# Performance work log

Hardware: AMD Instinct MI355X
Metric: run time of the kernel (lower is better)

## Reference

```python
import jax, jax.numpy as jnp
import numpy as np

N, E, DIN, H, CHID, COUT, S = 20000, 320000, 128, 4, 64, 64, 32
EPS_BN = 1e-5


def setup_inputs() -> dict:
    key = jax.random.key(0)
    ks = jax.random.split(key, 20)
    g = lambda k, shp, s=0.1: jax.random.normal(k, shp, dtype=jnp.float32) * s
    return {
        "x": jax.random.normal(ks[0], (N, DIN), dtype=jnp.float32),
        "edge_index": jax.random.randint(ks[1], (2, E), 0, N, dtype=jnp.int32),
        "struct_feat": jax.random.normal(ks[2], (N, S), dtype=jnp.float32),
        # GATConv (layer 1)
        "W1": g(ks[3], (H * CHID, DIN)),
        "att_src1": g(ks[4], (1, H, CHID)),
        "att_dst1": g(ks[5], (1, H, CHID)),
        "bias1": jnp.zeros((CHID,), jnp.float32),
        # HybridGateGATLayer (layer 2)
        "W2": g(ks[6], (H * COUT, CHID)),
        "att_src2": g(ks[7], (1, H, COUT)),
        "att_dst2": g(ks[8], (1, H, COUT)),
        "bias2": jnp.zeros((COUT,), jnp.float32),
        "Wt": g(ks[9], (1, S)),
        "bt": jnp.zeros((1,), jnp.float32),
        "We1": g(ks[10], (8, 4), 0.5),
        "be1": jnp.zeros((8,), jnp.float32),
        "We2": g(ks[11], (1, 8), 0.5),
        "be2": jnp.zeros((1,), jnp.float32),
        "betas": jnp.array([1.15, 0.85, 0.1, 0.08, 0.12], jnp.float32),
    }


def _seg_softmax(logits, seg, n):
    m = jax.ops.segment_max(logits, seg, num_segments=n)
    m = jnp.where(jnp.isfinite(m), m, 0.0)
    ex = jnp.exp(logits - m[seg])
    s = jax.ops.segment_sum(ex, seg, num_segments=n)
    return ex / (s[seg] + 1e-16)


def _cos(a, b):
    na = jnp.maximum(jnp.linalg.norm(a, axis=-1), 1e-8)
    nb = jnp.maximum(jnp.linalg.norm(b, axis=-1), 1e-8)
    return (a * b).sum(-1) / (na * nb)


def reference(x, edge_index, struct_feat, W1, att_src1, att_dst1, bias1,
              W2, att_src2, att_dst2, bias2, Wt, bt, We1, be1, We2, be2, betas):
    n = x.shape[0]
    src0, dst0 = edge_index[0], edge_index[1]
    # ---- layer 1: standard GATConv with self loops, concat=False (head mean) ----
    loop = jnp.arange(n, dtype=src0.dtype)
    src = jnp.concatenate([src0, loop])
    dst = jnp.concatenate([dst0, loop])
    h = (x @ W1.T).reshape(n, H, CHID)
    a_s = (h * att_src1).sum(-1)  # [N,H]
    a_d = (h * att_dst1).sum(-1)
    al = jax.nn.leaky_relu(a_s[src] + a_d[dst], 0.2)  # [E+N,H]
    alpha1 = _seg_softmax(al, dst, n)
    out1 = jax.ops.segment_sum(h[src] * alpha1[..., None], dst, num_segments=n)
    h1 = jax.nn.relu(out1.mean(1) + bias1)  # [N,CHID]
    # batch norm (affine=False, batch stats, biased var)
    mu = h1.mean(0)
    var = ((h1 - mu) ** 2).mean(0)
    h1 = (h1 - mu) / jnp.sqrt(var + EPS_BN)
    # ---- layer 2: HybridGateGATLayer (no self loops) ----
    x2 = (h1 @ W2.T).reshape(n, H, COUT)
    node_trust = jax.nn.sigmoid(struct_feat @ Wt.T + bt).squeeze(-1)  # [N]
    as2 = (x2 * att_src2).sum(-1)
    ad2 = (x2 * att_dst2).sum(-1)
    j, i = src0, dst0
    alpha_raw = jax.nn.leaky_relu(as2[j] + ad2[i], 0.2)  # [E,H]
    struct_sim = _cos(struct_feat[j], struct_feat[i])  # [E]
    xf = x2.reshape(n, H * COUT)
    feat_sim = _cos(xf[j], xf[i])
    agreement = struct_sim * feat_sim
    conflict = jnp.abs(struct_sim - feat_sim)
    cues = jnp.stack([struct_sim, feat_sim, agreement, conflict], axis=-1)  # [E,4]
    gate = (jax.nn.relu(cues @ We1.T + be1) @ We2.T + be2).squeeze(-1)
    edge_bonus = jax.nn.sigmoid(gate) * jax.nn.relu(agreement)
    edge_trust = jnp.sqrt(jnp.clip(node_trust[j] * node_trust[i], 0.0))
    trust_bonus = edge_trust * jax.nn.relu(0.5 * (struct_sim + feat_sim))
    gate_logit = (betas[0] * struct_sim + betas[1] * feat_sim + betas[2] * agreement
                  + betas[3] * edge_bonus + betas[4] * trust_bonus)
    alpha2 = _seg_softmax(alpha_raw + gate_logit[:, None], i, n)  # [E,H]
    out2 = jax.ops.segment_sum(x2[j] * alpha2[..., None], i, num_segments=n)
    return out2.mean(1) + bias2  # [N,COUT]
```

## Files before the change

kernel.cpp:

```cpp
#include <hip/hip_runtime.h>
#include <hip/hip_bf16.h>
#include <hip/hip_fp16.h>

#define C_DIN 128
#define C_H 4
#define C_CH 64
#define C_HC 256
#define C_S 32
#define ACH 32
#define MBLK 64
#define XROW 264

typedef __attribute__((ext_vector_type(8))) _Float16 half8;
typedef __attribute__((ext_vector_type(4))) float f32x4;

__device__ __forceinline__ float lrelu(float x) { return x >= 0.f ? x : 0.2f * x; }

__device__ __forceinline__ float sub_sum32(float v) {
#pragma unroll
    for (int off = 16; off > 0; off >>= 1) v += __shfl_xor(v, off);
    return v;
}

__global__ void k_count(const int* __restrict__ dst, int* __restrict__ deg, int E) {
    int e = blockIdx.x * blockDim.x + threadIdx.x;
    if (e < E) atomicAdd(&deg[dst[e]], 1);
}

__global__ void k_scan(const int* __restrict__ deg, int* __restrict__ row_ptr,
                       int* __restrict__ cursor, int n) {
    __shared__ int part[1024];
    int t = threadIdx.x;
    const int C = (n + 1023) / 1024;
    int base = t * C;
    int s = 0;
    for (int k = 0; k < C; ++k) {
        int idx = base + k;
        if (idx < n) s += deg[idx];
    }
    part[t] = s;
    __syncthreads();
    for (int off = 1; off < 1024; off <<= 1) {
        int v = (t >= off) ? part[t - off] : 0;
        __syncthreads();
        part[t] += v;
        __syncthreads();
    }
    int run = (t == 0) ? 0 : part[t - 1];
    for (int k = 0; k < C; ++k) {
        int idx = base + k;
        if (idx < n) { row_ptr[idx] = run; cursor[idx] = run; run += deg[idx]; }
    }
    if (t == 1023) row_ptr[n] = run;
}

__global__ void k_scatter(const int* __restrict__ src, const int* __restrict__ dst,
                          int* __restrict__ cursor, int* __restrict__ adj_src, int E) {
    int e = blockIdx.x * blockDim.x + threadIdx.x;
    if (e < E) {
        int d = dst[e];
        int p = atomicAdd(&cursor[d], 1);
        adj_src[p] = src[e];
    }
}

__global__ __launch_bounds__(256) void k_gemm1(
    const float* __restrict__ x, const float* __restrict__ W1,
    const float* __restrict__ att_s, const float* __restrict__ att_d,
    __half* __restrict__ hh_out, float* __restrict__ a_s, float* __restrict__ a_d, int n) {
    __shared__ __align__(16) _Float16 bs[4 * 16 * 64 * 8];
    __shared__ __align__(16) _Float16 as_[4 * 4 * 64 * 8];
    int t = threadIdx.x;
    int r0 = blockIdx.x * MBLK;
    {
        int c = t;
        const float4* wrow = (const float4*)(W1 + (size_t)c * C_DIN);
        int nt = c >> 4, cl = c & 15;
#pragma unroll
        for (int ch = 0; ch < 16; ++ch) {
            float4 f0 = wrow[ch * 2], f1 = wrow[ch * 2 + 1];
            int ks = ch >> 2, lg = ch & 3;
            _Float16* dst = &bs[(((ks * 16 + nt) * 64) + (lg * 16 + cl)) * 8];
            dst[0] = (_Float16)f0.x; dst[1] = (_Float16)f0.y;
            dst[2] = (_Float16)f0.z; dst[3] = (_Float16)f0.w;
            dst[4] = (_Float16)f1.x; dst[5] = (_Float16)f1.y;
            dst[6] = (_Float16)f1.z; dst[7] = (_Float16)f1.w;
        }
    }
    {
        int row = t >> 2, q = t & 3;
        int rr = r0 + row;
        int mt = row >> 4, rl = row & 15;
        const float4* xrow = (const float4*)(x + (size_t)rr * C_DIN);
#pragma unroll
        for (int cc = 0; cc < 4; ++cc) {
            int ch = q * 4 + cc;
            float4 f0 = make_float4(0, 0, 0, 0), f1 = make_float4(0, 0, 0, 0);
            if (rr < n) { f0 = xrow[ch * 2]; f1 = xrow[ch * 2 + 1]; }
            int ks = ch >> 2, lg = ch & 3;
            _Float16* dst = &as_[(((ks * 4 + mt) * 64) + (lg * 16 + rl)) * 8];
            dst[0] = (_Float16)f0.x; dst[1] = (_Float16)f0.y;
            dst[2] = (_Float16)f0.z; dst[3] = (_Float16)f0.w;
            dst[4] = (_Float16)f1.x; dst[5] = (_Float16)f1.y;
            dst[6] = (_Float16)f1.z; dst[7] = (_Float16)f1.w;
        }
    }
    __syncthreads();
    int w = t >> 6, l = t & 63;
    f32x4 acc[4][4];
#pragma unroll
    for (int mt = 0; mt < 4; ++mt)
#pragma unroll
        for (int nt = 0; nt < 4; ++nt) acc[mt][nt] = (f32x4){0.f, 0.f, 0.f, 0.f};
#pragma unroll
    for (int ks = 0; ks < 4; ++ks) {
        half8 af[4], bf[4];
#pragma unroll
        for (int mt = 0; mt < 4; ++mt)
            af[mt] = *(const half8*)&as_[(((ks * 4 + mt) * 64) + l) * 8];
#pragma unroll
        for (int nt = 0; nt < 4; ++nt)
            bf[nt] = *(const half8*)&bs[(((ks * 16 + (w * 4 + nt)) * 64) + l) * 8];
#pragma unroll
        for (int mt = 0; mt < 4; ++mt)
#pragma unroll
            for (int nt = 0; nt < 4; ++nt)
                acc[mt][nt] = __builtin_amdgcn_mfma_f32_16x16x32_f16(af[mt], bf[nt],
                                                                     acc[mt][nt], 0, 0, 0);
    }
    int cl = l & 15, rg = l >> 4;
    float atv_s[4], atv_d[4];
#pragma unroll
    for (int nt = 0; nt < 4; ++nt) {
        atv_s[nt] = att_s[w * 64 + nt * 16 + cl];
        atv_d[nt] = att_d[w * 64 + nt * 16 + cl];
    }
#pragma unroll
    for (int mt = 0; mt < 4; ++mt) {
#pragma unroll
        for (int r = 0; r < 4; ++r) {
            int rr = r0 + mt * 16 + rg * 4 + r;
            float vs = 0.f, vd = 0.f;
#pragma unroll
            for (int nt = 0; nt < 4; ++nt) {
                float v = acc[mt][nt][r];
                vs += atv_s[nt] * v;
                vd += atv_d[nt] * v;
                if (rr < n)
                    hh_out[(size_t)rr * C_HC + w * 64 + nt * 16 + cl] = __float2half(v);
            }
#pragma unroll
            for (int off = 1; off < 16; off <<= 1) {
                vs += __shfl_xor(vs, off);
                vd += __shfl_xor(vd, off);
            }
            if (cl == 0 && rr < n) { a_s[rr * C_H + w] = vs; a_d[rr * C_H + w] = vd; }
        }
    }
}

__global__ void k_layer1(const int* __restrict__ row_ptr, const int* __restrict__ adj_src,
                         const __half* __restrict__ hhlf, const float* __restrict__ a_s,
                         const float* __restrict__ a_d, const float* __restrict__ bias1,
                         float* __restrict__ h1) {
    int d = blockIdx.x;
    int t = threadIdx.x, hh = t >> 5, cp = t & 31;
    int beg = row_ptr[d], end = row_ptr[d + 1];
    float adh = a_d[d * C_H + hh];
    float p_self = expf(lrelu(a_s[d * C_H + hh] + adh));
    __shared__ float alpha_l[C_H][ACH];
    __shared__ int src_l[ACH];
    const __half2* selfrow = (const __half2*)(hhlf + (size_t)d * C_HC + hh * 64);
    float2 sv = __half22float2(selfrow[cp]);
    float accx = p_self * sv.x, accy = p_self * sv.y;
    float s_part = (cp == 0) ? p_self : 0.f;
    for (int cbeg = beg; cbeg < end; cbeg += ACH) {
        int cn = min(end - cbeg, ACH);
        __syncthreads();
        if (cp < cn) {
            int s = adj_src[cbeg + cp];
            if (hh == 0) src_l[cp] = s;
            float p = expf(lrelu(a_s[s * C_H + hh] + adh));
            alpha_l[hh][cp] = p;
            s_part += p;
        }
        __syncthreads();
        for (int i = 0; i < cn; ++i) {
            int s = src_l[i];
            float a = alpha_l[hh][i];
            float2 v = __half22float2(
                *(const __half2*)(hhlf + (size_t)s * C_HC + hh * 64 + cp * 2));
            accx += a * v.x;
            accy += a * v.y;
        }
    }
    float s = sub_sum32(s_part);
    float inv = 1.f / (s + 1e-16f);
    __shared__ float2 red[128];
    red[t] = make_float2(accx * inv, accy * inv);
    __syncthreads();
    if (t < 32) {
        float2 r0 = red[t], r1 = red[t + 32], r2 = red[t + 64], r3 = red[t + 96];
        float2 b = *(const float2*)&bias1[t * 2];
        float vx = (r0.x + r1.x + r2.x + r3.x) * 0.25f + b.x;
        float vy = (r0.y + r1.y + r2.y + r3.y) * 0.25f + b.y;
        *(float2*)&h1[(size_t)d * C_CH + t * 2] =
            make_float2(fmaxf(vx, 0.f), fmaxf(vy, 0.f));
    }
}

__global__ void k_bnstats(const float* __restrict__ h1, float* __restrict__ bn, int n) {
    int t = threadIdx.x;
    int c = t & 63, rg = t >> 6;
    float s = 0.f, s2 = 0.f;
    for (int r = blockIdx.x * 4 + rg; r < n; r += gridDim.x * 4) {
        float v = h1[(size_t)r * C_CH + c];
        s += v;
        s2 += v * v;
    }
    __shared__ float ls[256], ls2[256];
    ls[t] = s; ls2[t] = s2;
    __syncthreads();
    if (t < 64) {
        s = ls[t] + ls[t + 64] + ls[t + 128] + ls[t + 192];
        s2 = ls2[t] + ls2[t + 64] + ls2[t + 128] + ls2[t + 192];
        atomicAdd(&bn[c], s);
        atomicAdd(&bn[64 + c], s2);
    }
}

__global__ __launch_bounds__(256) void k_gemm2(
    const float* __restrict__ h1, const float* __restrict__ W2,
    const float* __restrict__ att_s, const float* __restrict__ att_d,
    const float* __restrict__ bn, __half* __restrict__ x2h,
    float* __restrict__ as2, float* __restrict__ ad2, float* __restrict__ nf, int n) {
    __shared__ __align__(16) _Float16 bs[2 * 16 * 64 * 8];
    __shared__ __align__(16) _Float16 as_[2 * 4 * 64 * 8];
    __shared__ float nq[64][4];
    int t = threadIdx.x;
    int r0 = blockIdx.x * MBLK;
    {
        int c = t;
        const float4* wrow = (const float4*)(W2 + (size_t)c * C_CH);
        int nt = c >> 4, cl = c & 15;
#pragma unroll
        for (int ch = 0; ch < 8; ++ch) {
            float4 f0 = wrow[ch * 2], f1 = wrow[ch * 2 + 1];
            int ks = ch >> 2, lg = ch & 3;
            _Float16* dst = &bs[(((ks * 16 + nt) * 64) + (lg * 16 + cl)) * 8];
            dst[0] = (_Float16)f0.x; dst[1] = (_Float16)f0.y;
            dst[2] = (_Float16)f0.z; dst[3] = (_Float16)f0.w;
            dst[4] = (_Float16)f1.x; dst[5] = (_Float16)f1.y;
            dst[6] = (_Float16)f1.z; dst[7] = (_Float16)f1.w;
        }
    }
    {
        int row = t >> 2, q = t & 3;
        int rr = r0 + row;
        int mt = row >> 4, rl = row & 15;
        const float invN = 1.f / (float)n;
        const float4* hrow = (const float4*)(h1 + (size_t)rr * C_CH);
#pragma unroll
        for (int cc = 0; cc < 2; ++cc) {
            int ch = q * 2 + cc;
            float4 f0 = make_float4(0, 0, 0, 0), f1 = make_float4(0, 0, 0, 0);
            if (rr < n) { f0 = hrow[ch * 2]; f1 = hrow[ch * 2 + 1]; }
            float4 s0 = *(const float4*)&bn[ch * 8];
            float4 s1 = *(const float4*)&bn[ch * 8 + 4];
            float4 q0 = *(const float4*)&bn[64 + ch * 8];
            float4 q1 = *(const float4*)&bn[64 + ch * 8 + 4];
            float4 mu0 = make_float4(s0.x * invN, s0.y * invN, s0.z * invN, s0.w * invN);
            float4 mu1 = make_float4(s1.x * invN, s1.y * invN, s1.z * invN, s1.w * invN);
            float4 rs0 = make_float4(rsqrtf(q0.x * invN - mu0.x * mu0.x + 1e-5f),
                                     rsqrtf(q0.y * invN - mu0.y * mu0.y + 1e-5f),
                                     rsqrtf(q0.z * invN - mu0.z * mu0.z + 1e-5f),
                                     rsqrtf(q0.w * invN - mu0.w * mu0.w + 1e-5f));
            float4 rs1 = make_float4(rsqrtf(q1.x * invN - mu1.x * mu1.x + 1e-5f),
                                     rsqrtf(q1.y * invN - mu1.y * mu1.y + 1e-5f),
                                     rsqrtf(q1.z * invN - mu1.z * mu1.z + 1e-5f),
                                     rsqrtf(q1.w * invN - mu1.w * mu1.w + 1e-5f));
            int ks = ch >> 2, lg = ch & 3;
            _Float16* dst = &as_[(((ks * 4 + mt) * 64) + (lg * 16 + rl)) * 8];
            dst[0] = (_Float16)((f0.x - mu0.x) * rs0.x);
            dst[1] = (_Float16)((f0.y - mu0.y) * rs0.y);
            dst[2] = (_Float16)((f0.z - mu0.z) * rs0.z);
            dst[3] = (_Float16)((f0.w - mu0.w) * rs0.w);
            dst[4] = (_Float16)((f1.x - mu1.x) * rs1.x);
            dst[5] = (_Float16)((f1.y - mu1.y) * rs1.y);
            dst[6] = (_Float16)((f1.z - mu1.z) * rs1.z);
            dst[7] = (_Float16)((f1.w - mu1.w) * rs1.w);
        }
    }
    __syncthreads();
    int w = t >> 6, l = t & 63;
    f32x4 acc[4][4];
#pragma unroll
    for (int mt = 0; mt < 4; ++mt)
#pragma unroll
        for (int nt = 0; nt < 4; ++nt) acc[mt][nt] = (f32x4){0.f, 0.f, 0.f, 0.f};
#pragma unroll
    for (int ks = 0; ks < 2; ++ks) {
        half8 af[4], bf[4];
#pragma unroll
        for (int mt = 0; mt < 4; ++mt)
            af[mt] = *(const half8*)&as_[(((ks * 4 + mt) * 64) + l) * 8];
#pragma unroll
        for (int nt = 0; nt < 4; ++nt)
            bf[nt] = *(const half8*)&bs[(((ks * 16 + (w * 4 + nt)) * 64) + l) * 8];
#pragma unroll
        for (int mt = 0; mt < 4; ++mt)
#pragma unroll
            for (int nt = 0; nt < 4; ++nt)
                acc[mt][nt] = __builtin_amdgcn_mfma_f32_16x16x32_f16(af[mt], bf[nt],
                                                                     acc[mt][nt], 0, 0, 0);
    }
    int cl = l & 15, rg = l >> 4;
    float atv_s[4], atv_d[4];
#pragma unroll
    for (int nt = 0; nt < 4; ++nt) {
        atv_s[nt] = att_s[w * 64 + nt * 16 + cl];
        atv_d[nt] = att_d[w * 64 + nt * 16 + cl];
    }
#pragma unroll
    for (int mt = 0; mt < 4; ++mt) {
#pragma unroll
        for (int r = 0; r < 4; ++r) {
            int rr = r0 + mt * 16 + rg * 4 + r;
            float vs = 0.f, vd = 0.f, vq = 0.f;
#pragma unroll
            for (int nt = 0; nt < 4; ++nt) {
                float v = acc[mt][nt][r];
                vs += atv_s[nt] * v;
                vd += atv_d[nt] * v;
                vq += v * v;
                if (rr < n)
                    x2h[(size_t)rr * C_HC + w * 64 + nt * 16 + cl] = __float2half(v);
            }
#pragma unroll
            for (int off = 1; off < 16; off <<= 1) {
                vs += __shfl_xor(vs, off);
                vd += __shfl_xor(vd, off);
                vq += __shfl_xor(vq, off);
            }
            if (cl == 0 && rr < n) {
                as2[rr * C_H + w] = vs;
                ad2[rr * C_H + w] = vd;
                nq[mt * 16 + rg * 4 + r][w] = vq;
            }
        }
    }
    __syncthreads();
    if (t < MBLK) {
        int rr = r0 + t;
        if (rr < n) {
            float qq = nq[t][0] + nq[t][1] + nq[t][2] + nq[t][3];
            nf[rr] = fmaxf(sqrtf(qq), 1e-8f);
        }
    }
}

__global__ void k_trust(const float* __restrict__ sf, const float* __restrict__ Wt,
                        const float* __restrict__ bt, float* __restrict__ trust,
                        float* __restrict__ ns, int n) {
    int i = blockIdx.x * blockDim.x + threadIdx.x;
    if (i >= n) return;
    const float4* r4 = (const float4*)(sf + (size_t)i * C_S);
    const float4* w4 = (const float4*)Wt;
    float d = 0.f, q = 0.f;
#pragma unroll
    for (int k = 0; k < 8; ++k) {
        float4 a = r4[k], w = w4[k];
        d += a.x * w.x + a.y * w.y + a.z * w.z + a.w * w.w;
        q += a.x * a.x + a.y * a.y + a.z * a.z + a.w * a.w;
    }
    trust[i] = 1.f / (1.f + expf(-(d + bt[0])));
    ns[i] = fmaxf(sqrtf(q), 1e-8f);
}

__global__ __launch_bounds__(128) void k_fused2(
    const int* __restrict__ row_ptr, const int* __restrict__ adj_src,
    const float* __restrict__ sf, const __half* __restrict__ x2h,
    const float* __restrict__ ns, const float* __restrict__ nf,
    const float* __restrict__ trust, const float* __restrict__ as2,
    const float* __restrict__ ad2, const float* __restrict__ We1,
    const float* __restrict__ be1, const float* __restrict__ We2,
    const float* __restrict__ be2, const float* __restrict__ betas,
    const float* __restrict__ bias2, float* __restrict__ out) {
    __shared__ __align__(16) _Float16 xrows[ACH * XROW];
    __shared__ __align__(16) _Float16 xd[C_HC];
    __shared__ float sfd[C_S];
    __shared__ float pbuf[C_H][ACH];
    __shared__ float2 red[128];
    int d = blockIdx.x;
    int t = threadIdx.x, hh = t >> 5, cp = t & 31;
    int beg = row_ptr[d], end = row_ptr[d + 1];
    if (t < 32) {
        ((float4*)xd)[t] = ((const float4*)(x2h + (size_t)d * C_HC))[t];
    } else if (t < 40) {
        ((float4*)sfd)[t - 32] = ((const float4*)(sf + (size_t)d * C_S))[t - 32];
    }
    float4 ad2d = *(const float4*)&ad2[d * C_H];
    float nsd = ns[d], nfd = nf[d], trd = trust[d];
    int er = t >> 2, q = t & 3;
    float accx = 0.f, accy = 0.f, s_part = 0.f;
    for (int cbeg = beg; cbeg < end; cbeg += ACH) {
        int cn = min(end - cbeg, ACH);
        __syncthreads();
        int sload = 0;
        if (q == 0 && er < cn) sload = adj_src[cbeg + er];
        int j = __shfl(sload, (t & 63) & ~3);
        if (er < cn) {
            const float4* grow = (const float4*)(x2h + (size_t)j * C_HC) + q * 8;
            float4* lrow = (float4*)&xrows[er * XROW + q * 64];
#pragma unroll
            for (int u = 0; u < 8; ++u) lrow[u] = grow[u];
        }
        __syncthreads();
        float fd = 0.f, sd = 0.f;
        if (er < cn) {
            const _Float16* xr = &xrows[er * XROW];
#pragma unroll
            for (int m = 0; m < 32; ++m) {
                float2 a = __half22float2(*(const __half2*)&xr[m * 8 + q * 2]);
                float2 b = __half22float2(*(const __half2*)&xd[m * 8 + q * 2]);
                fd += a.x * b.x + a.y * b.y;
            }
            const float4* sj = (const float4*)(sf + (size_t)j * C_S) + q * 2;
#pragma unroll
            for (int u = 0; u < 2; ++u) {
                float4 a = sj[u];
                float4 b = *(const float4*)&sfd[q * 8 + u * 4];
                sd += a.x * b.x + a.y * b.y + a.z * b.z + a.w * b.w;
            }
        }
        fd += __shfl_xor(fd, 1); fd += __shfl_xor(fd, 2);
        sd += __shfl_xor(sd, 1); sd += __shfl_xor(sd, 2);
        if (q == 0 && er < cn) {
            float ss = sd / (nsd * ns[j]);
            float fs = fd / (nfd * nf[j]);
            float agr = ss * fs;
            float con = fabsf(ss - fs);
            float gate = be2[0];
#pragma unroll
            for (int o = 0; o < 8; ++o) {
                float hdn = We1[o * 4 + 0] * ss + We1[o * 4 + 1] * fs +
                            We1[o * 4 + 2] * agr + We1[o * 4 + 3] * con + be1[o];
                gate += We2[o] * fmaxf(hdn, 0.f);
            }
            float eb = (1.f / (1.f + expf(-gate))) * fmaxf(agr, 0.f);
            float et = sqrtf(fmaxf(trd * trust[j], 0.f));
            float tb = et * fmaxf(0.5f * (ss + fs), 0.f);
            float g = betas[0] * ss + betas[1] * fs + betas[2] * agr +
                      betas[3] * eb + betas[4] * tb;
            float4 asj = *(const float4*)&as2[j * C_H];
            pbuf[0][er] = expf(lrelu(asj.x + ad2d.x) + g);
            pbuf[1][er] = expf(lrelu(asj.y + ad2d.y) + g);
            pbuf[2][er] = expf(lrelu(asj.z + ad2d.z) + g);
            pbuf[3][er] = expf(lrelu(asj.w + ad2d.w) + g);
        }
        __syncthreads();
        for (int i = 0; i < cn; ++i) {
            float pv = pbuf[hh][i];
            float2 v = __half22float2(
                *(const __half2*)&xrows[i * XROW + hh * 64 + cp * 2]);
            accx += pv * v.x;
            accy += pv * v.y;
        }
        if (cp < cn) s_part += pbuf[hh][cp];
    }
    float s = sub_sum32(s_part);
    float inv = 1.f / (s + 1e-16f);
    red[t] = make_float2(accx * inv, accy * inv);
    __syncthreads();
    if (t < 32) {
        float2 r0 = red[t], r1 = red[t + 32], r2 = red[t + 64], r3 = red[t + 96];
        float2 b = *(const float2*)&bias2[t * 2];
        float vx = (r0.x + r1.x + r2.x + r3.x) * 0.25f + b.x;
        float vy = (r0.y + r1.y + r2.y + r3.y) * 0.25f + b.y;
        *(float2*)&out[(size_t)d * C_CH + t * 2] = make_float2(vx, vy);
    }
}

static inline size_t al256(size_t x) { return (x + 255) & ~(size_t)255; }

extern "C" void kernel_launch(void* const* d_in, const int* in_sizes, int n_in,
                              void* d_out, int out_size, void* d_ws, size_t ws_size,
                              hipStream_t stream) {
    const float* x      = (const float*)d_in[0];
    const int*   ei     = (const int*)d_in[1];
    const float* sf     = (const float*)d_in[2];
    const float* W1     = (const float*)d_in[3];
    const float* atts1  = (const float*)d_in[4];
    const float* attd1  = (const float*)d_in[5];
    const float* bias1  = (const float*)d_in[6];
    const float* W2     = (const float*)d_in[7];
    const float* atts2  = (const float*)d_in[8];
    const float* attd2  = (const float*)d_in[9];
    const float* bias2  = (const float*)d_in[10];
    const float* Wt     = (const float*)d_in[11];
    const float* bt     = (const float*)d_in[12];
    const float* We1    = (const float*)d_in[13];
    const float* be1    = (const float*)d_in[14];
    const float* We2    = (const float*)d_in[15];
    const float* be2    = (const float*)d_in[16];
    const float* betas  = (const float*)d_in[17];

    const int N = in_sizes[0] / C_DIN;
    const int E = in_sizes[1] / 2;
    const int* srcs = ei;
    const int* dsts = ei + E;

    char* p = (char*)d_ws;
    size_t off = 0;
    auto take = [&](size_t bytes) { char* r = p + off; off = al256(off + bytes); return r; };
    __half* hhlf  = (__half*)take((size_t)N * C_HC * 2);
    float* h1     = (float*)take((size_t)N * C_CH * 4);
    float* a_s1   = (float*)take((size_t)N * C_H * 4);
    float* a_d1   = (float*)take((size_t)N * C_H * 4);
    float* nf     = (float*)take((size_t)N * 4);
    float* ns     = (float*)take((size_t)N * 4);
    float* trust  = (float*)take((size_t)N * 4);
    int*   deg    = (int*)take((size_t)N * 4);
    int*   rowp   = (int*)take((size_t)(N + 1) * 4);
    int*   cursor = (int*)take((size_t)N * 4);
    int*   adj_s  = (int*)take((size_t)E * 4);
    float* bn     = (float*)take(128 * 4);
    (void)ws_size;
    __half* x2h = hhlf;
    float* as2  = a_s1;
    float* ad2  = a_d1;

    hipMemsetAsync(deg, 0, (size_t)N * 4, stream);
    hipMemsetAsync(bn, 0, 128 * 4, stream);

    k_count<<<(E + 255) / 256, 256, 0, stream>>>(dsts, deg, E);
    k_scan<<<1, 1024, 0, stream>>>(deg, rowp, cursor, N);
    k_scatter<<<(E + 255) / 256, 256, 0, stream>>>(srcs, dsts, cursor, adj_s, E);

    k_gemm1<<<(N + MBLK - 1) / MBLK, 256, 0, stream>>>(x, W1, atts1, attd1, hhlf, a_s1, a_d1, N);
    k_layer1<<<N, 128, 0, stream>>>(rowp, adj_s, hhlf, a_s1, a_d1, bias1, h1);
    k_bnstats<<<128, 256, 0, stream>>>(h1, bn, N);

    k_gemm2<<<(N + MBLK - 1) / MBLK, 256, 0, stream>>>(h1, W2, atts2, attd2, bn, x2h,
                                                       as2, ad2, nf, N);
    k_trust<<<(N + 255) / 256, 256, 0, stream>>>(sf, Wt, bt, trust, ns, N);
    k_fused2<<<N, 128, 0, stream>>>(rowp, adj_s, sf, x2h, ns, nf, trust, as2, ad2,
                                    We1, be1, We2, be2, betas, bias2, (float*)d_out);
}
```

Measured before the change: 311.5 us.

## Drop LDS staging of neighbor rows; read x2 rows directly from global memory

Removes the shared-memory buffer that staged each chunk's gathered neighbor feature rows. Each thread now computes the feature dot product straight from global loads, and the destination row is kept in registers instead of LDS. The aggregation loop re-reads neighbor rows from global memory (expected to hit cache) using source indices stored in a small shared array. This cuts LDS footprint and LDS traffic, which can raise occupancy, but it doubles global gather traffic, adds an extra barrier per chunk, and puts a dependent global load inside the serial aggregation loop.

```diff
diff --git a/kernel.cpp b/kernel.cpp
--- a/kernel.cpp
+++ b/kernel.cpp
@@ -9,7 +9,6 @@
 #define C_S 32
 #define ACH 32
 #define MBLK 64
-#define XROW 264
 
 typedef __attribute__((ext_vector_type(8))) _Float16 half8;
 typedef __attribute__((ext_vector_type(4))) float f32x4;
@@ -386,50 +385,49 @@
     const float* __restrict__ be1, const float* __restrict__ We2,
     const float* __restrict__ be2, const float* __restrict__ betas,
     const float* __restrict__ bias2, float* __restrict__ out) {
-    __shared__ __align__(16) _Float16 xrows[ACH * XROW];
-    __shared__ __align__(16) _Float16 xd[C_HC];
-    __shared__ float sfd[C_S];
+    __shared__ int js[ACH];
     __shared__ float pbuf[C_H][ACH];
     __shared__ float2 red[128];
     int d = blockIdx.x;
     int t = threadIdx.x, hh = t >> 5, cp = t & 31;
+    int er = t >> 2, q = t & 3;
     int beg = row_ptr[d], end = row_ptr[d + 1];
-    if (t < 32) {
-        ((float4*)xd)[t] = ((const float4*)(x2h + (size_t)d * C_HC))[t];
-    } else if (t < 40) {
-        ((float4*)sfd)[t - 32] = ((const float4*)(sf + (size_t)d * C_S))[t - 32];
+    float4 xdreg[8], sfdreg[2];
+    {
+        const float4* dr = (const float4*)(x2h + (size_t)d * C_HC + q * 64);
+#pragma unroll
+        for (int u = 0; u < 8; ++u) xdreg[u] = dr[u];
+        const float4* sr = (const float4*)(sf + (size_t)d * C_S + q * 8);
+        sfdreg[0] = sr[0]; sfdreg[1] = sr[1];
     }
     float4 ad2d = *(const float4*)&ad2[d * C_H];
     float nsd = ns[d], nfd = nf[d], trd = trust[d];
-    int er = t >> 2, q = t & 3;
     float accx = 0.f, accy = 0.f, s_part = 0.f;
     for (int cbeg = beg; cbeg < end; cbeg += ACH) {
         int cn = min(end - cbeg, ACH);
         __syncthreads();
-        int sload = 0;
-        if (q == 0 && er < cn) sload = adj_src[cbeg + er];
-        int j = __shfl(sload, (t & 63) & ~3);
+        if (q == 0 && er < cn) js[er] = adj_src[cbeg + er];
+        __syncthreads();
+        float fd = 0.f, sd = 0.f;
+        int j = 0;
         if (er < cn) {
-            const float4* grow = (const float4*)(x2h + (size_t)j * C_HC) + q * 8;
-            float4* lrow = (float4*)&xrows[er * XROW + q * 64];
-#pragma unroll
-            for (int u = 0; u < 8; ++u) lrow[u] = grow[u];
-        }
-        __syncthreads();
-        float fd = 0.f, sd = 0.f;
-        if (er < cn) {
-            const _Float16* xr = &xrows[er * XROW];
-#pragma unroll
-            for (int m = 0; m < 32; ++m) {
-                float2 a = __half22float2(*(const __half2*)&xr[m * 8 + q * 2]);
-                float2 b = __half22float2(*(const __half2*)&xd[m * 8 + q * 2]);
-                fd += a.x * b.x + a.y * b.y;
-            }
-            const float4* sj = (const float4*)(sf + (size_t)j * C_S) + q * 2;
+            j = js[er];
+            const float4* grow = (const float4*)(x2h + (size_t)j * C_HC + q * 64);
+#pragma unroll
+            for (int u = 0; u < 8; ++u) {
+                float4 a4 = grow[u];
+                const __half2* pa = (const __half2*)&a4;
+                const __half2* pb = (const __half2*)&xdreg[u];
+#pragma unroll
+                for (int k = 0; k < 4; ++k) {
+                    float2 a = __half22float2(pa[k]), b = __half22float2(pb[k]);
+                    fd += a.x * b.x + a.y * b.y;
+                }
+            }
+            const float4* sj = (const float4*)(sf + (size_t)j * C_S + q * 8);
 #pragma unroll
             for (int u = 0; u < 2; ++u) {
-                float4 a = sj[u];
-                float4 b = *(const float4*)&sfd[q * 8 + u * 4];
+                float4 a = sj[u], b = sfdreg[u];
                 sd += a.x * b.x + a.y * b.y + a.z * b.z + a.w * b.w;
             }
         }
@@ -460,9 +458,10 @@
         }
         __syncthreads();
         for (int i = 0; i < cn; ++i) {
+            int jj = js[i];
             float pv = pbuf[hh][i];
             float2 v = __half22float2(
-                *(const __half2*)&xrows[i * XROW + hh * 64 + cp * 2]);
+                *(const __half2*)(x2h + (size_t)jj * C_HC + hh * 64 + cp * 2));
             accx += pv * v.x;
             accy += pv * v.y;
         }
```

New measurement: 340.5 us. 1.09x slower.
